# Kernel optimization log

Measured on AMD Instinct MI355X. Metric: run time of the kernel, lower is better.

Reference implementation:

```python
import jax, jax.numpy as jnp
import numpy as np

N_EMBD = 1024
N_HEAD = 16
HEAD_DIM = N_EMBD // N_HEAD


def setup_inputs() -> dict:
    key = jax.random.key(0)
    k1, k2, k3 = jax.random.split(key, 3)
    x = jax.random.normal(k1, (4, 2048, N_EMBD), dtype=jnp.float32)
    w_qkv = jax.random.normal(k2, (N_EMBD, 3 * N_EMBD), dtype=jnp.float32) * (N_EMBD ** -0.5)
    w_proj = jax.random.normal(k3, (N_EMBD, N_EMBD), dtype=jnp.float32) * (N_EMBD ** -0.5)
    return {"x": x, "w_qkv": w_qkv, "w_proj": w_proj}


def reference(x, w_qkv, w_proj):
    B, T, C = x.shape
    qkv = jnp.einsum('btc,cd->btd', x, w_qkv)  # [B,T,3C]
    q, k, v = jnp.split(qkv, 3, axis=-1)
    def heads(t):
        return t.reshape(B, T, N_HEAD, HEAD_DIM).transpose(0, 2, 1, 3)  # [B,H,T,D]
    q, k, v = heads(q), heads(k), heads(v)
    scale = 1.0 / jnp.sqrt(jnp.asarray(HEAD_DIM, dtype=x.dtype))
    att = jnp.einsum('bhqd,bhkd->bhqk', q, k) * scale  # [B,H,T,T]
    causal = jnp.tril(jnp.ones((T, T), dtype=bool))
    att = jnp.where(causal[None, None], att, jnp.asarray(-jnp.inf, dtype=att.dtype))
    att = jax.nn.softmax(att, axis=-1)
    out = jnp.einsum('bhqk,bhkd->bhqd', att, v)  # [B,H,T,D]
    out = out.transpose(0, 2, 1, 3).reshape(B, T, C)
    return jnp.einsum('btc,cd->btd', out, w_proj)
```

## Files before the change

kernel.cpp:

```cpp
#include <hip/hip_runtime.h>
#include <cstdint>
#include <cstddef>
#include <type_traits>

typedef float  f32x4   __attribute__((ext_vector_type(4)));
typedef __bf16 bf16x8  __attribute__((ext_vector_type(8)));
typedef short  short4_t __attribute__((ext_vector_type(4)));
typedef short  short8_t __attribute__((ext_vector_type(8)));

__device__ __forceinline__ short f2bf(float f) {
  return __builtin_bit_cast(short, (__bf16)f);
}

__device__ __forceinline__ void gl_lds16(const void* g, void* l) {
  __builtin_amdgcn_global_load_lds((const __attribute__((address_space(1))) void*)g,
                                   (__attribute__((address_space(3))) void*)l, 16, 0, 0);
}

__global__ void convert_bf16(const float* __restrict__ X, short* __restrict__ Xb) {
  int i = (blockIdx.x * 256 + threadIdx.x) * 4;
  f32x4 v = *(const f32x4*)&X[i];
  short4_t o;
#pragma unroll
  for (int j = 0; j < 4; j++) o[j] = f2bf(v[j]);
  *(short4_t*)&Xb[i] = o;
}

__global__ void transpose_bf16(const float* __restrict__ W, short* __restrict__ WT,
                               int K, int N) {
  __shared__ float tile[32][33];
  int tx = threadIdx.x & 31, ty = threadIdx.x >> 5;
  int n0 = blockIdx.x * 32, k0 = blockIdx.y * 32;
#pragma unroll
  for (int i = 0; i < 32; i += 8)
    tile[ty + i][tx] = W[(size_t)(k0 + ty + i) * N + n0 + tx];
  __syncthreads();
#pragma unroll
  for (int i = 0; i < 32; i += 8)
    WT[(size_t)(n0 + ty + i) * K + k0 + tx] = f2bf(tile[tx][ty + i]);
}

template <int MODE>
__global__ __launch_bounds__(256, 2) void gemm_bt(
    const short* __restrict__ A, const short* __restrict__ Bt,
    float* __restrict__ outf, short* __restrict__ Qo, short* __restrict__ Ko,
    short* __restrict__ Vo, int M, int N, int K) {
  __shared__ alignas(16) short As[128 * 32];
  __shared__ alignas(16) short Bs[128 * 32];
  const int tid = threadIdx.x;
  const int lane = tid & 63;
  const int g = lane & 15, q = lane >> 4;
  const int wave = tid >> 6;
  const int m0 = blockIdx.y * 128, n0 = blockIdx.x * 128;
  const int wm = (wave >> 1) * 64, wn = (wave & 1) * 64;

  const int srow = tid >> 2;
  const int scol = (tid & 3) * 8;
  const short* ap0 = A  + (size_t)(m0 + srow) * K + scol;
  const short* ap1 = A  + (size_t)(m0 + 64 + srow) * K + scol;
  const short* bp0 = Bt + (size_t)(n0 + srow) * K + scol;
  const short* bp1 = Bt + (size_t)(n0 + 64 + srow) * K + scol;
  short* la0 = &As[tid * 8];
  short* la1 = &As[(tid + 256) * 8];
  short* lb0 = &Bs[tid * 8];
  short* lb1 = &Bs[(tid + 256) * 8];

  f32x4 acc[4][4] = {};

  for (int k0 = 0; k0 < K; k0 += 32) {
    __syncthreads();
    gl_lds16(ap0 + k0, la0);
    gl_lds16(ap1 + k0, la1);
    gl_lds16(bp0 + k0, lb0);
    gl_lds16(bp1 + k0, lb1);
    __syncthreads();
    bf16x8 af[4], bfr[4];
#pragma unroll
    for (int mt = 0; mt < 4; mt++)
      af[mt] = *(const bf16x8*)&As[(wm + mt * 16 + g) * 32 + q * 8];
#pragma unroll
    for (int nt = 0; nt < 4; nt++)
      bfr[nt] = *(const bf16x8*)&Bs[(wn + nt * 16 + g) * 32 + q * 8];
#pragma unroll
    for (int mt = 0; mt < 4; mt++)
#pragma unroll
      for (int nt = 0; nt < 4; nt++)
        acc[mt][nt] = __builtin_amdgcn_mfma_f32_16x16x32_bf16(af[mt], bfr[nt],
                                                              acc[mt][nt], 0, 0, 0);
  }

  if (MODE == 0) {
#pragma unroll
    for (int mt = 0; mt < 4; mt++)
#pragma unroll
      for (int nt = 0; nt < 4; nt++) {
        int n = n0 + wn + nt * 16 + g;
        int mbase = m0 + wm + mt * 16 + q * 4;
#pragma unroll
        for (int r = 0; r < 4; r++)
          outf[(size_t)(mbase + r) * N + n] = acc[mt][nt][r];
      }
  } else {
#pragma unroll
    for (int nt = 0; nt < 4; nt++) {
      int n = n0 + wn + nt * 16 + g;
      int which = n >> 10;
      int c = n & 1023;
      int h = c >> 6, d = c & 63;
#pragma unroll
      for (int mt = 0; mt < 4; mt++) {
        int mbase = m0 + wm + mt * 16 + q * 4;
        int b = mbase >> 11, t = mbase & 2047;
        if (which == 2) {
          short4_t pv;
#pragma unroll
          for (int r = 0; r < 4; r++) pv[r] = f2bf(acc[mt][nt][r]);
          *(short4_t*)&Vo[((size_t)((b << 4) + h) * 64 + d) * 2048 + t] = pv;
        } else {
          short* dst = (which == 0) ? Qo : Ko;
#pragma unroll
          for (int r = 0; r < 4; r++)
            dst[((size_t)((b << 4) + h) * 2048 + (t + r)) * 64 + d] =
                f2bf(acc[mt][nt][r]);
        }
      }
    }
  }
}

__global__ __launch_bounds__(256, 2) void attn_fwd(
    const short* __restrict__ Qg, const short* __restrict__ Kg,
    const short* __restrict__ Vt, short* __restrict__ Og) {
  __shared__ alignas(16) short Ps[4][32 * 136];
  __shared__ alignas(16) short Ks[128 * 72];
  __shared__ alignas(16) short VTs[64 * 136];

  const int tid = threadIdx.x, lane = tid & 63, wave = tid >> 6;
  const int g = lane & 15, q = lane >> 4;
  const int bh = blockIdx.y;
  const size_t base = (size_t)bh * (2048 * 64);
  const int b = bh >> 4, h = bh & 15;
  const float cs = 0.18033688011f;

  short8_t kreg[4], vreg[4];
  auto loadKV = [&](int kt) {
    const short* Kp  = Kg + base + (size_t)kt * 128 * 64;
    const short* Vtp = Vt + base + (size_t)kt * 128;
#pragma unroll
    for (int i = 0; i < 4; i++) {
      int c = tid + i * 256;
      kreg[i] = *(const short8_t*)&Kp[(c >> 3) * 64 + (c & 7) * 8];
      vreg[i] = *(const short8_t*)&Vtp[(size_t)(c >> 4) * 2048 + (c & 15) * 8];
    }
  };
  auto storeKV = [&]() {
#pragma unroll
    for (int i = 0; i < 4; i++) {
      int c = tid + i * 256;
      *(short8_t*)&Ks[(c >> 3) * 72 + (c & 7) * 8] = kreg[i];
      *(short8_t*)&VTs[(c >> 4) * 136 + (c & 15) * 8] = vreg[i];
    }
  };

  for (int half = 0; half < 2; half++) {
    const int qt = (half == 0) ? (int)blockIdx.x : 15 - (int)blockIdx.x;

    __syncthreads();
    {
      const short* Qp = Qg + base + (size_t)qt * 128 * 64;
      short* Qs = &Ps[0][0];
#pragma unroll
      for (int i = 0; i < 4; i++) {
        int c = tid + i * 256;
        *(short8_t*)&Qs[(c >> 3) * 72 + (c & 7) * 8] =
            *(const short8_t*)&Qp[(c >> 3) * 64 + (c & 7) * 8];
      }
    }
    __syncthreads();
    bf16x8 bq[2][2];
#pragma unroll
    for (int nt = 0; nt < 2; nt++)
#pragma unroll
      for (int kk = 0; kk < 2; kk++) {
        bf16x8 v = *(const bf16x8*)&Ps[0][(wave * 32 + nt * 16 + g) * 72 + kk * 32 + q * 8];
#pragma unroll
        for (int j = 0; j < 8; j++) v[j] = (__bf16)((float)v[j] * cs);
        bq[nt][kk] = v;
      }

    f32x4 ot[4][2] = {};
    float m_run[2] = {-1e30f, -1e30f};
    float l_run[2] = {0.0f, 0.0f};

    auto compute = [&](auto diagc, int kt) {
      constexpr bool DIAG = decltype(diagc)::value;
      f32x4 st[8][2] = {};
#pragma unroll
      for (int kk = 0; kk < 2; kk++)
#pragma unroll
        for (int mt = 0; mt < 8; mt++) {
          bf16x8 ak = *(const bf16x8*)&Ks[(mt * 16 + g) * 72 + kk * 32 + q * 8];
#pragma unroll
          for (int nt = 0; nt < 2; nt++)
            st[mt][nt] = __builtin_amdgcn_mfma_f32_16x16x32_bf16(ak, bq[nt][kk],
                                                                 st[mt][nt], 0, 0, 0);
        }

#pragma unroll
      for (int nt = 0; nt < 2; nt++) {
        const int qloc = wave * 32 + nt * 16 + g;
        float tmax = -1e30f;
#pragma unroll
        for (int mt = 0; mt < 8; mt++)
#pragma unroll
          for (int r = 0; r < 4; r++) {
            if (DIAG) {
              if (mt * 16 + q * 4 + r > qloc) st[mt][nt][r] = -1e30f;
            }
            tmax = fmaxf(tmax, st[mt][nt][r]);
          }
        tmax = fmaxf(tmax, __shfl_xor(tmax, 16));
        tmax = fmaxf(tmax, __shfl_xor(tmax, 32));
        const float mnew = fmaxf(m_run[nt], tmax);
        const float alpha = __builtin_amdgcn_exp2f(m_run[nt] - mnew);
        float psum = 0.0f;
        short* Pw = &Ps[wave][0];
#pragma unroll
        for (int mt = 0; mt < 8; mt++) {
          short4_t pk;
#pragma unroll
          for (int r = 0; r < 4; r++) {
            float p = __builtin_amdgcn_exp2f(st[mt][nt][r] - mnew);
            psum += p;
            pk[r] = f2bf(p);
          }
          *(short4_t*)&Pw[(nt * 16 + g) * 136 + mt * 16 + q * 4] = pk;
        }
        psum += __shfl_xor(psum, 16);
        psum += __shfl_xor(psum, 32);
        l_run[nt] = l_run[nt] * alpha + psum;
        m_run[nt] = mnew;
#pragma unroll
        for (int mt = 0; mt < 4; mt++) {
          ot[mt][nt][0] *= alpha; ot[mt][nt][1] *= alpha;
          ot[mt][nt][2] *= alpha; ot[mt][nt][3] *= alpha;
        }
      }

#pragma unroll
      for (int kk = 0; kk < 4; kk++) {
        bf16x8 pb[2];
#pragma unroll
        for (int nt = 0; nt < 2; nt++)
          pb[nt] = *(const bf16x8*)&Ps[wave][(nt * 16 + g) * 136 + kk * 32 + q * 8];
#pragma unroll
        for (int mt = 0; mt < 4; mt++) {
          bf16x8 av = *(const bf16x8*)&VTs[(mt * 16 + g) * 136 + kk * 32 + q * 8];
#pragma unroll
          for (int nt = 0; nt < 2; nt++)
            ot[mt][nt] = __builtin_amdgcn_mfma_f32_16x16x32_bf16(av, pb[nt],
                                                                 ot[mt][nt], 0, 0, 0);
        }
      }
    };

    loadKV(0);
    for (int kt = 0; kt < qt; kt++) {
      __syncthreads();
      storeKV();
      loadKV(kt + 1);
      __syncthreads();
      compute(std::integral_constant<bool, false>{}, kt);
    }
    __syncthreads();
    storeKV();
    __syncthreads();
    compute(std::integral_constant<bool, true>{}, qt);

#pragma unroll
    for (int nt = 0; nt < 2; nt++) {
      const float inv = 1.0f / l_run[nt];
      const int qrow = qt * 128 + wave * 32 + nt * 16 + g;
      size_t obase = ((size_t)b * 2048 + qrow) * 1024 + h * 64;
#pragma unroll
      for (int mt = 0; mt < 4; mt++) {
        short4_t ov;
#pragma unroll
        for (int r = 0; r < 4; r++) ov[r] = f2bf(ot[mt][nt][r] * inv);
        *(short4_t*)&Og[obase + mt * 16 + q * 4] = ov;
      }
    }
  }
}

extern "C" void kernel_launch(void* const* d_in, const int* in_sizes, int n_in,
                              void* d_out, int out_size, void* d_ws, size_t ws_size,
                              hipStream_t stream) {
  const float* x      = (const float*)d_in[0];
  const float* w_qkv  = (const float*)d_in[1];
  const float* w_proj = (const float*)d_in[2];
  float* out = (float*)d_out;

  char* ws = (char*)d_ws;
  short* xb     = (short*)(ws);
  short* wqkvT  = (short*)(ws + 16777216);
  short* wprojT = (short*)(ws + 23068672);
  short* Qb     = (short*)(ws + 25165824);
  short* Kb     = (short*)(ws + 41943040);
  short* Vtb    = (short*)(ws + 58720256);

  convert_bf16<<<8192, 256, 0, stream>>>(x, xb);
  {
    dim3 gq(96, 32); transpose_bf16<<<gq, 256, 0, stream>>>(w_qkv, wqkvT, 1024, 3072);
    dim3 gp(32, 32); transpose_bf16<<<gp, 256, 0, stream>>>(w_proj, wprojT, 1024, 1024);
  }
  {
    dim3 g(24, 64);
    gemm_bt<1><<<g, 256, 0, stream>>>(xb, wqkvT, nullptr, Qb, Kb, Vtb, 8192, 3072, 1024);
  }
  {
    dim3 g(8, 64);
    attn_fwd<<<g, 256, 0, stream>>>(Qb, Kb, Vtb, xb );
  }
  {
    dim3 g(8, 64);
    gemm_bt<0><<<g, 256, 0, stream>>>(xb, wprojT, out, nullptr, nullptr, nullptr,
                                      8192, 1024, 1024);
  }
}
```

Measured before the change: 259.0 us.

## Fuse x conversion into QKV GEMM, restage epilogue, rework attention scheduling

Drops the separate fp32-to-bf16 pass over x: the QKV GEMM now loads fp32 A through registers, converts it, and double-buffers the global loads into LDS in place of global_load_lds. Q/K outputs are staged through LDS so they are written as coalesced 16-byte rows. Attention launches one block per query tile, heaviest tiles first, instead of pairing tiles per block. It keeps Q in registers, shrinks the P buffer to half-width chunks and raises occupancy hints. The trade-offs are higher register pressure, more LDS for the GEMM epilogue, and loss of the asynchronous LDS-load path.

Measured after the change: 320.3 us. +23.7%, slower.

```diff
diff --git a/kernel.cpp b/kernel.cpp
--- a/kernel.cpp
+++ b/kernel.cpp
@@ -3,27 +3,13 @@
 #include <cstddef>
 #include <type_traits>
 
-typedef float  f32x4   __attribute__((ext_vector_type(4)));
-typedef __bf16 bf16x8  __attribute__((ext_vector_type(8)));
+typedef float  f32x4    __attribute__((ext_vector_type(4)));
+typedef __bf16 bf16x8   __attribute__((ext_vector_type(8)));
 typedef short  short4_t __attribute__((ext_vector_type(4)));
 typedef short  short8_t __attribute__((ext_vector_type(8)));
 
 __device__ __forceinline__ short f2bf(float f) {
   return __builtin_bit_cast(short, (__bf16)f);
-}
-
-__device__ __forceinline__ void gl_lds16(const void* g, void* l) {
-  __builtin_amdgcn_global_load_lds((const __attribute__((address_space(1))) void*)g,
-                                   (__attribute__((address_space(3))) void*)l, 16, 0, 0);
-}
-
-__global__ void convert_bf16(const float* __restrict__ X, short* __restrict__ Xb) {
-  int i = (blockIdx.x * 256 + threadIdx.x) * 4;
-  f32x4 v = *(const f32x4*)&X[i];
-  short4_t o;
-#pragma unroll
-  for (int j = 0; j < 4; j++) o[j] = f2bf(v[j]);
-  *(short4_t*)&Xb[i] = o;
 }
 
 __global__ void transpose_bf16(const float* __restrict__ W, short* __restrict__ WT,
@@ -40,39 +26,65 @@
     WT[(size_t)(n0 + ty + i) * K + k0 + tx] = f2bf(tile[tx][ty + i]);
 }
 
-template <int MODE>
-__global__ __launch_bounds__(256, 2) void gemm_bt(
-    const short* __restrict__ A, const short* __restrict__ Bt,
+template <int MODE, bool AF32>
+__global__ __launch_bounds__(256, 4) void gemm_bt(
+    const void* __restrict__ Av, const short* __restrict__ Bt,
     float* __restrict__ outf, short* __restrict__ Qo, short* __restrict__ Ko,
     short* __restrict__ Vo, int M, int N, int K) {
-  __shared__ alignas(16) short As[128 * 32];
-  __shared__ alignas(16) short Bs[128 * 32];
+  constexpr int SMEM = (MODE == 1) ? (128 * 136 * 2) : 16384;
+  __shared__ alignas(16) char smem[SMEM];
+  short* As = (short*)smem;
+  short* Bs = (short*)(smem + 8192);
+
   const int tid = threadIdx.x;
-  const int lane = tid & 63;
+  const int lane = tid & 63, wave = tid >> 6;
   const int g = lane & 15, q = lane >> 4;
-  const int wave = tid >> 6;
   const int m0 = blockIdx.y * 128, n0 = blockIdx.x * 128;
   const int wm = (wave >> 1) * 64, wn = (wave & 1) * 64;
 
   const int srow = tid >> 2;
   const int scol = (tid & 3) * 8;
-  const short* ap0 = A  + (size_t)(m0 + srow) * K + scol;
-  const short* ap1 = A  + (size_t)(m0 + 64 + srow) * K + scol;
-  const short* bp0 = Bt + (size_t)(n0 + srow) * K + scol;
-  const short* bp1 = Bt + (size_t)(n0 + 64 + srow) * K + scol;
-  short* la0 = &As[tid * 8];
-  short* la1 = &As[(tid + 256) * 8];
-  short* lb0 = &Bs[tid * 8];
-  short* lb1 = &Bs[(tid + 256) * 8];
+  const float* Af = (const float*)Av;
+  const short* Ab = (const short*)Av;
+
+  f32x4    raf[4];
+  short8_t ra[2], rb[2];
+
+  auto load_regs = [&](int k0) {
+    if constexpr (AF32) {
+      const float* p0 = &Af[(size_t)(m0 + srow) * K + k0 + scol];
+      const float* p1 = &Af[(size_t)(m0 + 64 + srow) * K + k0 + scol];
+      raf[0] = *(const f32x4*)p0; raf[1] = *(const f32x4*)(p0 + 4);
+      raf[2] = *(const f32x4*)p1; raf[3] = *(const f32x4*)(p1 + 4);
+    } else {
+      ra[0] = *(const short8_t*)&Ab[(size_t)(m0 + srow) * K + k0 + scol];
+      ra[1] = *(const short8_t*)&Ab[(size_t)(m0 + 64 + srow) * K + k0 + scol];
+    }
+    rb[0] = *(const short8_t*)&Bt[(size_t)(n0 + srow) * K + k0 + scol];
+    rb[1] = *(const short8_t*)&Bt[(size_t)(n0 + 64 + srow) * K + k0 + scol];
+  };
+  auto store_regs = [&]() {
+    short8_t w0, w1;
+    if constexpr (AF32) {
+#pragma unroll
+      for (int j = 0; j < 4; j++) {
+        w0[j] = f2bf(raf[0][j]); w0[4 + j] = f2bf(raf[1][j]);
+        w1[j] = f2bf(raf[2][j]); w1[4 + j] = f2bf(raf[3][j]);
+      }
+    } else { w0 = ra[0]; w1 = ra[1]; }
+    *(short8_t*)&As[tid * 8] = w0;
+    *(short8_t*)&As[(tid + 256) * 8] = w1;
+    *(short8_t*)&Bs[tid * 8] = rb[0];
+    *(short8_t*)&Bs[(tid + 256) * 8] = rb[1];
+  };
 
   f32x4 acc[4][4] = {};
-
-  for (int k0 = 0; k0 < K; k0 += 32) {
+  const int KB = K >> 5;
+  load_regs(0);
+  for (int kb = 0; kb < KB; kb++) {
     __syncthreads();
-    gl_lds16(ap0 + k0, la0);
-    gl_lds16(ap1 + k0, la1);
-    gl_lds16(bp0 + k0, lb0);
-    gl_lds16(bp1 + k0, lb1);
+    store_regs();
+    if (kb + 1 < KB) load_regs((kb + 1) << 5);
     __syncthreads();
     bf16x8 af[4], bfr[4];
 #pragma unroll
@@ -101,46 +113,76 @@
           outf[(size_t)(mbase + r) * N + n] = acc[mt][nt][r];
       }
   } else {
-#pragma unroll
-    for (int nt = 0; nt < 4; nt++) {
-      int n = n0 + wn + nt * 16 + g;
-      int which = n >> 10;
-      int c = n & 1023;
-      int h = c >> 6, d = c & 63;
-#pragma unroll
-      for (int mt = 0; mt < 4; mt++) {
-        int mbase = m0 + wm + mt * 16 + q * 4;
-        int b = mbase >> 11, t = mbase & 2047;
-        if (which == 2) {
+    const int which = n0 >> 10;
+    const int b = m0 >> 11;
+    if (which == 2) {
+#pragma unroll
+      for (int nt = 0; nt < 4; nt++) {
+        int c = (n0 + wn + nt * 16 + g) & 1023;
+        int h = c >> 6, d = c & 63;
+#pragma unroll
+        for (int mt = 0; mt < 4; mt++) {
+          int t = (m0 + wm + mt * 16 + q * 4) & 2047;
           short4_t pv;
 #pragma unroll
           for (int r = 0; r < 4; r++) pv[r] = f2bf(acc[mt][nt][r]);
           *(short4_t*)&Vo[((size_t)((b << 4) + h) * 64 + d) * 2048 + t] = pv;
-        } else {
-          short* dst = (which == 0) ? Qo : Ko;
+        }
+      }
+    } else {
+      __syncthreads();
+      short* Cs = (short*)smem;
+#pragma unroll
+      for (int mt = 0; mt < 4; mt++)
+#pragma unroll
+        for (int nt = 0; nt < 4; nt++)
 #pragma unroll
           for (int r = 0; r < 4; r++)
-            dst[((size_t)((b << 4) + h) * 2048 + (t + r)) * 64 + d] =
+            Cs[(wm + mt * 16 + q * 4 + r) * 136 + wn + nt * 16 + g] =
                 f2bf(acc[mt][nt][r]);
-        }
-      }
-    }
-  }
-}
-
-__global__ __launch_bounds__(256, 2) void attn_fwd(
+      __syncthreads();
+      short* dst = (which == 0) ? Qo : Ko;
+      const int h0 = (n0 & 1023) >> 6;
+      const int trow = tid >> 1, half = tid & 1;
+      const int t = (m0 + trow) & 2047;
+      const size_t gb = ((size_t)((b << 4) + h0 + half) * 2048 + t) * 64;
+#pragma unroll
+      for (int j = 0; j < 8; j++)
+        *(short8_t*)&dst[gb + j * 8] =
+            *(const short8_t*)&Cs[trow * 136 + half * 64 + j * 8];
+    }
+  }
+}
+
+__global__ __launch_bounds__(256, 3) void attn_fwd(
     const short* __restrict__ Qg, const short* __restrict__ Kg,
     const short* __restrict__ Vt, short* __restrict__ Og) {
-  __shared__ alignas(16) short Ps[4][32 * 136];
   __shared__ alignas(16) short Ks[128 * 72];
   __shared__ alignas(16) short VTs[64 * 136];
+  __shared__ alignas(16) short Ps[4][32 * 72];
 
   const int tid = threadIdx.x, lane = tid & 63, wave = tid >> 6;
   const int g = lane & 15, q = lane >> 4;
-  const int bh = blockIdx.y;
+  const int id = blockIdx.x;
+  const int bh = id & 63;
+  const int qt = 15 - (id >> 6);
   const size_t base = (size_t)bh * (2048 * 64);
   const int b = bh >> 4, h = bh & 15;
   const float cs = 0.18033688011f;
+
+  bf16x8 bq[2][2];
+  {
+    const short* Qp = Qg + base + (size_t)qt * 128 * 64;
+#pragma unroll
+    for (int nt = 0; nt < 2; nt++)
+#pragma unroll
+      for (int kk = 0; kk < 2; kk++) {
+        bf16x8 v = *(const bf16x8*)&Qp[(wave * 32 + nt * 16 + g) * 64 + kk * 32 + q * 8];
+#pragma unroll
+        for (int j = 0; j < 8; j++) v[j] = (__bf16)((float)v[j] * cs);
+        bq[nt][kk] = v;
+      }
+  }
 
   short8_t kreg[4], vreg[4];
   auto loadKV = [&](int kt) {
@@ -162,97 +204,78 @@
     }
   };
 
-  for (int half = 0; half < 2; half++) {
-    const int qt = (half == 0) ? (int)blockIdx.x : 15 - (int)blockIdx.x;
-
-    __syncthreads();
-    {
-      const short* Qp = Qg + base + (size_t)qt * 128 * 64;
-      short* Qs = &Ps[0][0];
-#pragma unroll
-      for (int i = 0; i < 4; i++) {
-        int c = tid + i * 256;
-        *(short8_t*)&Qs[(c >> 3) * 72 + (c & 7) * 8] =
-            *(const short8_t*)&Qp[(c >> 3) * 64 + (c & 7) * 8];
-      }
-    }
-    __syncthreads();
-    bf16x8 bq[2][2];
-#pragma unroll
-    for (int nt = 0; nt < 2; nt++)
-#pragma unroll
-      for (int kk = 0; kk < 2; kk++) {
-        bf16x8 v = *(const bf16x8*)&Ps[0][(wave * 32 + nt * 16 + g) * 72 + kk * 32 + q * 8];
-#pragma unroll
-        for (int j = 0; j < 8; j++) v[j] = (__bf16)((float)v[j] * cs);
-        bq[nt][kk] = v;
-      }
-
-    f32x4 ot[4][2] = {};
-    float m_run[2] = {-1e30f, -1e30f};
-    float l_run[2] = {0.0f, 0.0f};
-
-    auto compute = [&](auto diagc, int kt) {
-      constexpr bool DIAG = decltype(diagc)::value;
-      f32x4 st[8][2] = {};
-#pragma unroll
-      for (int kk = 0; kk < 2; kk++)
-#pragma unroll
-        for (int mt = 0; mt < 8; mt++) {
-          bf16x8 ak = *(const bf16x8*)&Ks[(mt * 16 + g) * 72 + kk * 32 + q * 8];
-#pragma unroll
-          for (int nt = 0; nt < 2; nt++)
-            st[mt][nt] = __builtin_amdgcn_mfma_f32_16x16x32_bf16(ak, bq[nt][kk],
-                                                                 st[mt][nt], 0, 0, 0);
+  f32x4 ot[4][2] = {};
+  float m_run[2] = {-1e30f, -1e30f};
+  float l_run[2] = {0.0f, 0.0f};
+
+  auto compute = [&](auto diagc) {
+    constexpr bool DIAG = decltype(diagc)::value;
+    f32x4 st[8][2] = {};
+#pragma unroll
+    for (int kk = 0; kk < 2; kk++)
+#pragma unroll
+      for (int mt = 0; mt < 8; mt++) {
+        bf16x8 ak = *(const bf16x8*)&Ks[(mt * 16 + g) * 72 + kk * 32 + q * 8];
+#pragma unroll
+        for (int nt = 0; nt < 2; nt++)
+          st[mt][nt] = __builtin_amdgcn_mfma_f32_16x16x32_bf16(ak, bq[nt][kk],
+                                                               st[mt][nt], 0, 0, 0);
+      }
+
+    short4_t pk[8][2];
+#pragma unroll
+    for (int nt = 0; nt < 2; nt++) {
+      const int qloc = wave * 32 + nt * 16 + g;
+      float tmax = -1e30f;
+#pragma unroll
+      for (int mt = 0; mt < 8; mt++)
+#pragma unroll
+        for (int r = 0; r < 4; r++) {
+          if (DIAG) {
+            if (mt * 16 + q * 4 + r > qloc) st[mt][nt][r] = -1e30f;
+          }
+          tmax = fmaxf(tmax, st[mt][nt][r]);
         }
-
-#pragma unroll
-      for (int nt = 0; nt < 2; nt++) {
-        const int qloc = wave * 32 + nt * 16 + g;
-        float tmax = -1e30f;
-#pragma unroll
-        for (int mt = 0; mt < 8; mt++)
-#pragma unroll
-          for (int r = 0; r < 4; r++) {
-            if (DIAG) {
-              if (mt * 16 + q * 4 + r > qloc) st[mt][nt][r] = -1e30f;
-            }
-            tmax = fmaxf(tmax, st[mt][nt][r]);
-          }
-        tmax = fmaxf(tmax, __shfl_xor(tmax, 16));
-        tmax = fmaxf(tmax, __shfl_xor(tmax, 32));
-        const float mnew = fmaxf(m_run[nt], tmax);
-        const float alpha = __builtin_amdgcn_exp2f(m_run[nt] - mnew);
-        float psum = 0.0f;
-        short* Pw = &Ps[wave][0];
-#pragma unroll
-        for (int mt = 0; mt < 8; mt++) {
-          short4_t pk;
-#pragma unroll
-          for (int r = 0; r < 4; r++) {
-            float p = __builtin_amdgcn_exp2f(st[mt][nt][r] - mnew);
-            psum += p;
-            pk[r] = f2bf(p);
-          }
-          *(short4_t*)&Pw[(nt * 16 + g) * 136 + mt * 16 + q * 4] = pk;
+      tmax = fmaxf(tmax, __shfl_xor(tmax, 16));
+      tmax = fmaxf(tmax, __shfl_xor(tmax, 32));
+      const float mnew = fmaxf(m_run[nt], tmax);
+      const float alpha = __builtin_amdgcn_exp2f(m_run[nt] - mnew);
+      float psum = 0.0f;
+#pragma unroll
+      for (int mt = 0; mt < 8; mt++)
+#pragma unroll
+        for (int r = 0; r < 4; r++) {
+          float p = __builtin_amdgcn_exp2f(st[mt][nt][r] - mnew);
+          psum += p;
+          pk[mt][nt][r] = f2bf(p);
         }
-        psum += __shfl_xor(psum, 16);
-        psum += __shfl_xor(psum, 32);
-        l_run[nt] = l_run[nt] * alpha + psum;
-        m_run[nt] = mnew;
-#pragma unroll
-        for (int mt = 0; mt < 4; mt++) {
-          ot[mt][nt][0] *= alpha; ot[mt][nt][1] *= alpha;
-          ot[mt][nt][2] *= alpha; ot[mt][nt][3] *= alpha;
-        }
-      }
-
-#pragma unroll
-      for (int kk = 0; kk < 4; kk++) {
+      psum += __shfl_xor(psum, 16);
+      psum += __shfl_xor(psum, 32);
+      l_run[nt] = l_run[nt] * alpha + psum;
+      m_run[nt] = mnew;
+#pragma unroll
+      for (int mt = 0; mt < 4; mt++) {
+        ot[mt][nt][0] *= alpha; ot[mt][nt][1] *= alpha;
+        ot[mt][nt][2] *= alpha; ot[mt][nt][3] *= alpha;
+      }
+    }
+
+    short* Pw = &Ps[wave][0];
+#pragma unroll
+    for (int half = 0; half < 2; half++) {
+#pragma unroll
+      for (int nt = 0; nt < 2; nt++)
+#pragma unroll
+        for (int mh = 0; mh < 4; mh++)
+          *(short4_t*)&Pw[(nt * 16 + g) * 72 + mh * 16 + q * 4] =
+              pk[half * 4 + mh][nt];
+#pragma unroll
+      for (int kh = 0; kh < 2; kh++) {
+        const int kk = half * 2 + kh;
         bf16x8 pb[2];
 #pragma unroll
         for (int nt = 0; nt < 2; nt++)
-          pb[nt] = *(const bf16x8*)&Ps[wave][(nt * 16 + g) * 136 + kk * 32 + q * 8];
+          pb[nt] = *(const bf16x8*)&Pw[(nt * 16 + g) * 72 + kh * 32 + q * 8];
 #pragma unroll
         for (int mt = 0; mt < 4; mt++) {
           bf16x8 av = *(const bf16x8*)&VTs[(mt * 16 + g) * 136 + kk * 32 + q * 8];
@@ -262,33 +285,33 @@
                                                                  ot[mt][nt], 0, 0, 0);
         }
       }
-    };
-
-    loadKV(0);
-    for (int kt = 0; kt < qt; kt++) {
-      __syncthreads();
-      storeKV();
-      loadKV(kt + 1);
-      __syncthreads();
-      compute(std::integral_constant<bool, false>{}, kt);
-    }
+    }
+  };
+
+  loadKV(0);
+  for (int kt = 0; kt < qt; kt++) {
     __syncthreads();
     storeKV();
+    loadKV(kt + 1);
     __syncthreads();
-    compute(std::integral_constant<bool, true>{}, qt);
-
-#pragma unroll
-    for (int nt = 0; nt < 2; nt++) {
-      const float inv = 1.0f / l_run[nt];
-      const int qrow = qt * 128 + wave * 32 + nt * 16 + g;
-      size_t obase = ((size_t)b * 2048 + qrow) * 1024 + h * 64;
-#pragma unroll
-      for (int mt = 0; mt < 4; mt++) {
-        short4_t ov;
-#pragma unroll
-        for (int r = 0; r < 4; r++) ov[r] = f2bf(ot[mt][nt][r] * inv);
-        *(short4_t*)&Og[obase + mt * 16 + q * 4] = ov;
-      }
+    compute(std::integral_constant<bool, false>{});
+  }
+  __syncthreads();
+  storeKV();
+  __syncthreads();
+  compute(std::integral_constant<bool, true>{});
+
+#pragma unroll
+  for (int nt = 0; nt < 2; nt++) {
+    const float inv = 1.0f / l_run[nt];
+    const int qrow = qt * 128 + wave * 32 + nt * 16 + g;
+    size_t obase = ((size_t)b * 2048 + qrow) * 1024 + h * 64;
+#pragma unroll
+    for (int mt = 0; mt < 4; mt++) {
+      short4_t ov;
+#pragma unroll
+      for (int r = 0; r < 4; r++) ov[r] = f2bf(ot[mt][nt][r] * inv);
+      *(short4_t*)&Og[obase + mt * 16 + q * 4] = ov;
     }
   }
 }
@@ -302,29 +325,28 @@
   float* out = (float*)d_out;
 
   char* ws = (char*)d_ws;
-  short* xb     = (short*)(ws);
-  short* wqkvT  = (short*)(ws + 16777216);
-  short* wprojT = (short*)(ws + 23068672);
-  short* Qb     = (short*)(ws + 25165824);
-  short* Kb     = (short*)(ws + 41943040);
-  short* Vtb    = (short*)(ws + 58720256);
-
-  convert_bf16<<<8192, 256, 0, stream>>>(x, xb);
+  short* wqkvT  = (short*)(ws);
+  short* wprojT = (short*)(ws + 6291456);
+  short* Qb     = (short*)(ws + 8388608);
+  short* Kb     = (short*)(ws + 25165824);
+  short* Vtb    = (short*)(ws + 41943040);
+  short* Ob     = (short*)(ws + 58720256);
+
   {
     dim3 gq(96, 32); transpose_bf16<<<gq, 256, 0, stream>>>(w_qkv, wqkvT, 1024, 3072);
     dim3 gp(32, 32); transpose_bf16<<<gp, 256, 0, stream>>>(w_proj, wprojT, 1024, 1024);
   }
   {
     dim3 g(24, 64);
-    gemm_bt<1><<<g, 256, 0, stream>>>(xb, wqkvT, nullptr, Qb, Kb, Vtb, 8192, 3072, 1024);
+    gemm_bt<1, true><<<g, 256, 0, stream>>>(x, wqkvT, nullptr, Qb, Kb, Vtb,
+                                            8192, 3072, 1024);
+  }
+  {
+    attn_fwd<<<dim3(1024), 256, 0, stream>>>(Qb, Kb, Vtb, Ob);
   }
   {
     dim3 g(8, 64);
-    attn_fwd<<<g, 256, 0, stream>>>(Qb, Kb, Vtb, xb );
-  }
-  {
-    dim3 g(8, 64);
-    gemm_bt<0><<<g, 256, 0, stream>>>(xb, wprojT, out, nullptr, nullptr, nullptr,
-                                      8192, 1024, 1024);
-  }
-}
+    gemm_bt<0, false><<<g, 256, 0, stream>>>(Ob, wprojT, out, nullptr, nullptr,
+                                             nullptr, 8192, 1024, 1024);
+  }
+}
```
